# Kernel optimization log

Hardware: AMD Instinct MI355X
Metric: run time of the kernel (lower is better)

The kernel has to match this reference:

```python
import jax, jax.numpy as jnp
import numpy as np

N = 50000
E = 800000
D_IN = 256
D_H = 256


def setup_inputs() -> dict:
    key = jax.random.key(0)
    ks = jax.random.split(key, 8)
    x = jax.random.normal(ks[0], (N, D_IN), dtype=jnp.float32)
    W1 = jax.random.normal(ks[1], (D_H, D_IN), dtype=jnp.float32) * (1.0 / np.sqrt(D_IN))
    b1 = jnp.zeros((D_H,), dtype=jnp.float32)
    W2 = jax.random.normal(ks[2], (D_H, D_H), dtype=jnp.float32) * (1.0 / np.sqrt(D_H))
    b2 = jnp.zeros((D_H,), dtype=jnp.float32)
    gamma = jnp.ones((D_H,), dtype=jnp.float32)
    beta = jnp.zeros((D_H,), dtype=jnp.float32)
    adj_values = jax.random.uniform(ks[3], (E,), dtype=jnp.float32)
    rows = jax.random.randint(ks[4], (E,), 0, N, dtype=jnp.int64)
    cols = jax.random.randint(ks[5], (E,), 0, N, dtype=jnp.int64)
    adj_indices = jnp.stack([rows, cols], axis=0)
    return {"x": x, "W1": W1, "b1": b1, "W2": W2, "b2": b2,
            "gamma": gamma, "beta": beta, "adj_values": adj_values,
            "adj_indices": adj_indices}


def _spmm(adj_indices, adj_values, h, n):
    # out[i] = sum_j A[i, j] * h[j]; COO row=indices[0], col=indices[1]
    rows, cols = adj_indices[0], adj_indices[1]
    msgs = adj_values[:, None] * h[cols]          # [E, D]
    return jax.ops.segment_sum(msgs, rows, num_segments=n)


def _layernorm(h, gamma, beta, eps=1e-5):
    mu = jnp.mean(h, axis=-1, keepdims=True)
    var = jnp.var(h, axis=-1, keepdims=True)
    return (h - mu) * jax.lax.rsqrt(var + eps) * gamma + beta


def reference(x, W1, b1, W2, b2, gamma, beta, adj_values, adj_indices):
    n = x.shape[0]
    h = x @ W1.T + b1
    h = _spmm(adj_indices, adj_values, h, n)
    h = jax.nn.gelu(h, approximate=False)
    h = h @ W2.T + b2
    h = _spmm(adj_indices, adj_values, h, n)
    h = jax.nn.gelu(h, approximate=False)
    h = _layernorm(h + x[:, :h.shape[1]], gamma, beta)
    return h
```

## Files before the change

kernel.cpp:

```cpp
#include <hip/hip_runtime.h>
#include <math.h>

#define DH 256
#define CAP 64

typedef _Float16 f16x4 __attribute__((ext_vector_type(4)));
typedef _Float16 f16x8 __attribute__((ext_vector_type(8)));
typedef __fp16 fp16x2 __attribute__((ext_vector_type(2)));
typedef float f32x4 __attribute__((ext_vector_type(4)));

__device__ __forceinline__ float gelu_exact(float v) {
    return 0.5f * v * (1.0f + erff(v * 0.70710678118654752f));
}

__device__ __forceinline__ unsigned short f2h_bits(float f) {
    _Float16 h = (_Float16)f;
    return __builtin_bit_cast(unsigned short, h);
}

__device__ __forceinline__ _Float16 bits2h(unsigned short u) {
    return __builtin_bit_cast(_Float16, u);
}

__device__ __forceinline__ unsigned pk2h(float a, float b) {
    fp16x2 r = __builtin_amdgcn_cvt_pkrtz(a, b);
    return __builtin_bit_cast(unsigned, r);
}

__device__ __forceinline__ void async_copy16(const void* g, void* l) {
    __builtin_amdgcn_global_load_lds(
        (const __attribute__((address_space(1))) void*)g,
        (__attribute__((address_space(3))) void*)l, 16, 0, 0);
}

__global__ void prep_kernel(const float* __restrict__ W1, const float* __restrict__ W2,
                            unsigned short* __restrict__ W1h, unsigned short* __restrict__ W2h,
                            int* __restrict__ cnt, int n) {
    const int WV = DH * DH / 4;
    int gid = blockIdx.x * blockDim.x + threadIdx.x;
    if (gid < 2 * WV) {
        const float* src = (gid < WV) ? W1 : W2;
        unsigned short* dst = (gid < WV) ? W1h : W2h;
        int i = (gid < WV) ? gid : gid - WV;
        float4 v = *(const float4*)(src + (size_t)i * 4);
        uint2 o;
        o.x = pk2h(v.x, v.y);
        o.y = pk2h(v.z, v.w);
        *(uint2*)(dst + (size_t)i * 4) = o;
    } else {
        int i = (gid - 2 * WV) * 4;
        if (i < n) {
            int4 z = {0, 0, 0, 0};
            if (i + 4 <= n) *(int4*)(cnt + i) = z;
            else for (int k = i; k < n; ++k) cnt[k] = 0;
        }
    }
}

__global__ void bucket_kernel(const int* __restrict__ idx, const float* __restrict__ vals,
                              int* __restrict__ cnt, unsigned* __restrict__ cvb, int E) {
    int e = blockIdx.x * blockDim.x + threadIdx.x;
    if (e >= E) return;
    int r = idx[e];
    int c = idx[E + e];
    float v = vals[e];
    int p = atomicAdd(&cnt[r], 1);
    if (p < CAP) {
        cvb[(size_t)r * CAP + p] = ((unsigned)c << 16) | (unsigned)f2h_bits(v);
    }
}

template<bool AF32>
__global__ __launch_bounds__(512) void gemm_mfma_kernel(
        const void* __restrict__ Ap, const unsigned short* __restrict__ B,
        const float* __restrict__ bias, unsigned short* __restrict__ C, int M) {
    __shared__ char smem[49152];
    const int tid  = threadIdx.x;
    const int lane = tid & 63;
    const int wid  = tid >> 6;
    const int m0   = blockIdx.x * 128;
    const int wm   = wid >> 2;
    const int wn   = wid & 3;
    const int l15  = lane & 15, l4 = lane >> 4;

    auto stage = [&](int buf, int k0) {
        char* sA = smem + buf * 24576;
        char* sB = sA + 8192;
        {
            int t = tid;
            int row = t >> 2;
            int sw  = (t & 3) ^ (row & 3);
            int gra = m0 + row; if (gra >= M) gra = M - 1;
            if (AF32) {
                const float* a32 = (const float*)Ap + (size_t)gra * DH + k0 + sw * 8;
                float4 lo = *(const float4*)a32;
                float4 hi = *(const float4*)(a32 + 4);
                uint4 pk;
                pk.x = pk2h(lo.x, lo.y);
                pk.y = pk2h(lo.z, lo.w);
                pk.z = pk2h(hi.x, hi.y);
                pk.w = pk2h(hi.z, hi.w);
                *(uint4*)(sA + (size_t)t * 16) = pk;
            } else {
                async_copy16((const unsigned short*)Ap + (size_t)gra * DH + k0 + sw * 8,
                             sA + ((size_t)(wid * 64)) * 16);
            }
        }
        #pragma unroll
        for (int k = 0; k < 2; ++k) {
            int t = k * 512 + tid;
            int row = t >> 2;
            int sw  = (t & 3) ^ (row & 3);
            async_copy16(B + (size_t)row * DH + k0 + sw * 8,
                         sB + ((size_t)(k * 512 + wid * 64)) * 16);
        }
    };

    f32x4 acc[4][4] = {};

    stage(0, 0);
    __syncthreads();

    #pragma unroll
    for (int t = 0; t < 8; ++t) {
        if (t < 7) stage((t + 1) & 1, (t + 1) * 32);

        char* sA = smem + (t & 1) * 24576;
        char* sB = sA + 8192;
        f16x8 af[4], bfg[4];
        #pragma unroll
        for (int f = 0; f < 4; ++f) {
            int ra = wm * 64 + f * 16 + l15;
            int rb = wn * 64 + f * 16 + l15;
            int ca = (l4 ^ (ra & 3)) * 16;
            int cb = (l4 ^ (rb & 3)) * 16;
            af[f]  = *(const f16x8*)(sA + ra * 64 + ca);
            bfg[f] = *(const f16x8*)(sB + rb * 64 + cb);
        }
        #pragma unroll
        for (int fm = 0; fm < 4; ++fm)
            #pragma unroll
            for (int fn = 0; fn < 4; ++fn)
                acc[fm][fn] = __builtin_amdgcn_mfma_f32_16x16x32_f16(af[fm], bfg[fn], acc[fm][fn], 0, 0, 0);

        __syncthreads();
    }

    #pragma unroll
    for (int fn = 0; fn < 4; ++fn) {
        float bb = bias[wn * 64 + fn * 16 + l15];
        #pragma unroll
        for (int fm = 0; fm < 4; ++fm) {
            int mrow = m0 + wm * 64 + fm * 16 + l4 * 4;
            unsigned short* cp = C + (size_t)mrow * DH + wn * 64 + fn * 16 + l15;
            #pragma unroll
            for (int r = 0; r < 4; ++r) {
                if (mrow + r < M) cp[(size_t)r * DH] = f2h_bits(acc[fm][fn][r] + bb);
            }
        }
    }
}

template<int MODE>
__global__ __launch_bounds__(256) void spmm_kernel(
        const _Float16* __restrict__ h, const int* __restrict__ cnt,
        const unsigned* __restrict__ cvb, const float* __restrict__ xres,
        const float* __restrict__ gamma, const float* __restrict__ beta,
        void* __restrict__ outp, int n) {
    const int lane = threadIdx.x & 63;
    const int row = blockIdx.x * 4 + (threadIdx.x >> 6);
    if (row >= n) return;
    int deg = cnt[row]; if (deg > CAP) deg = CAP;
    const unsigned* cb = cvb + (size_t)row * CAP;

    f16x4 accA = {}, accB = {};
    int j = 0;
    for (; j + 4 <= deg; j += 4) {
        uint4 e = *(const uint4*)(cb + j);
        f16x4 p0 = *(const f16x4*)(h + (size_t)(e.x >> 16) * DH + lane * 4);
        f16x4 p1 = *(const f16x4*)(h + (size_t)(e.y >> 16) * DH + lane * 4);
        f16x4 p2 = *(const f16x4*)(h + (size_t)(e.z >> 16) * DH + lane * 4);
        f16x4 p3 = *(const f16x4*)(h + (size_t)(e.w >> 16) * DH + lane * 4);
        _Float16 v0 = bits2h((unsigned short)(e.x & 0xFFFFu));
        _Float16 v1 = bits2h((unsigned short)(e.y & 0xFFFFu));
        _Float16 v2 = bits2h((unsigned short)(e.z & 0xFFFFu));
        _Float16 v3 = bits2h((unsigned short)(e.w & 0xFFFFu));
        accA += p0 * v0; accB += p1 * v1;
        accA += p2 * v2; accB += p3 * v3;
    }
    for (; j < deg; ++j) {
        unsigned e = cb[j];
        f16x4 p0 = *(const f16x4*)(h + (size_t)(e >> 16) * DH + lane * 4);
        _Float16 v0 = bits2h((unsigned short)(e & 0xFFFFu));
        accA += p0 * v0;
    }

    float ax = (float)accA[0] + (float)accB[0];
    float ay = (float)accA[1] + (float)accB[1];
    float az = (float)accA[2] + (float)accB[2];
    float aw = (float)accA[3] + (float)accB[3];

    ax = gelu_exact(ax); ay = gelu_exact(ay); az = gelu_exact(az); aw = gelu_exact(aw);

    if (MODE == 1) {
        float4 xr = *(const float4*)(xres + (size_t)row * DH + lane * 4);
        ax += xr.x; ay += xr.y; az += xr.z; aw += xr.w;
        float s  = ax + ay + az + aw;
        float s2 = ax * ax + ay * ay + az * az + aw * aw;
        #pragma unroll
        for (int off = 32; off > 0; off >>= 1) {
            s  += __shfl_xor(s,  off);
            s2 += __shfl_xor(s2, off);
        }
        float mu  = s * (1.0f / 256.0f);
        float var = s2 * (1.0f / 256.0f) - mu * mu;
        float rs  = rsqrtf(var + 1e-5f);
        float4 g  = *(const float4*)(gamma + lane * 4);
        float4 bt = *(const float4*)(beta + lane * 4);
        float4 o;
        o.x = (ax - mu) * rs * g.x + bt.x;
        o.y = (ay - mu) * rs * g.y + bt.y;
        o.z = (az - mu) * rs * g.z + bt.z;
        o.w = (aw - mu) * rs * g.w + bt.w;
        *(float4*)((float*)outp + (size_t)row * DH + lane * 4) = o;
    } else {
        uint2 pk;
        pk.x = pk2h(ax, ay);
        pk.y = pk2h(az, aw);
        *(uint2*)((_Float16*)outp + (size_t)row * DH + lane * 4) = pk;
    }
}

extern "C" void kernel_launch(void* const* d_in, const int* in_sizes, int n_in,
                              void* d_out, int out_size, void* d_ws, size_t ws_size,
                              hipStream_t stream) {
    const float* x     = (const float*)d_in[0];
    const float* W1    = (const float*)d_in[1];
    const float* b1    = (const float*)d_in[2];
    const float* W2    = (const float*)d_in[3];
    const float* b2    = (const float*)d_in[4];
    const float* gamma = (const float*)d_in[5];
    const float* beta  = (const float*)d_in[6];
    const float* avals = (const float*)d_in[7];
    const int*   aidx  = (const int*)d_in[8];

    const int n = in_sizes[0] / DH;
    const int e = in_sizes[7];
    float* out = (float*)d_out;

    _Float16* g1h = (_Float16*)d_out;

    char* ws = (char*)d_ws;
    size_t off = 0;
    _Float16* hb = (_Float16*)(ws + off);              off += (size_t)n * DH * 2;
    off = (off + 255) & ~(size_t)255;
    unsigned short* W1h = (unsigned short*)(ws + off); off += (size_t)DH * DH * 2;
    off = (off + 255) & ~(size_t)255;
    unsigned short* W2h = (unsigned short*)(ws + off); off += (size_t)DH * DH * 2;
    off = (off + 255) & ~(size_t)255;
    int* cnt = (int*)(ws + off);                       off += (size_t)n * sizeof(int);
    off = (off + 255) & ~(size_t)255;
    unsigned* cvb = (unsigned*)(ws + off);             off += (size_t)n * CAP * sizeof(unsigned);

    const int gemm_gx = (n + 127) / 128;
    const int prep_items = 2 * (DH * DH / 4) + (n + 3) / 4;

    prep_kernel<<<(prep_items + 255) / 256, 256, 0, stream>>>(W1, W2, W1h, W2h, cnt, n);
    bucket_kernel<<<(e + 255) / 256, 256, 0, stream>>>(aidx, avals, cnt, cvb, e);

    gemm_mfma_kernel<true><<<gemm_gx, 512, 0, stream>>>(x, W1h, b1, (unsigned short*)hb, n);

    spmm_kernel<0><<<(n + 3) / 4, 256, 0, stream>>>(
        hb, cnt, cvb, nullptr, nullptr, nullptr, g1h, n);

    gemm_mfma_kernel<false><<<gemm_gx, 512, 0, stream>>>(g1h, W2h, b2, (unsigned short*)hb, n);

    spmm_kernel<1><<<(n + 3) / 4, 256, 0, stream>>>(
        hb, cnt, cvb, x, gamma, beta, out, n);
}
```

Measured before the change: 216.2 us.

## Drop prep kernel and LDS staging; load GEMM operands directly from global

Removes the separate prep kernel that converted W1/W2 to fp16 and zeroed the bucket counters. The counter zeroing moves into the first GEMM kernel, and the weights are now read as fp32 and converted inline. The GEMM also drops its double-buffered LDS staging and barriers, so each wave loads its A and B fragments straight from global memory into registers. This saves one launch and the LDS traffic, but every wave now reloads and reconverts fp32 weights with strided, partially coalesced global loads, and nothing overlaps those loads with the MFMA work.

After: 308.7 us. 42.8% more time.

```diff
diff --git a/kernel.cpp b/kernel.cpp
--- a/kernel.cpp
+++ b/kernel.cpp
@@ -25,36 +25,6 @@
 __device__ __forceinline__ unsigned pk2h(float a, float b) {
     fp16x2 r = __builtin_amdgcn_cvt_pkrtz(a, b);
     return __builtin_bit_cast(unsigned, r);
-}
-
-__device__ __forceinline__ void async_copy16(const void* g, void* l) {
-    __builtin_amdgcn_global_load_lds(
-        (const __attribute__((address_space(1))) void*)g,
-        (__attribute__((address_space(3))) void*)l, 16, 0, 0);
-}
-
-__global__ void prep_kernel(const float* __restrict__ W1, const float* __restrict__ W2,
-                            unsigned short* __restrict__ W1h, unsigned short* __restrict__ W2h,
-                            int* __restrict__ cnt, int n) {
-    const int WV = DH * DH / 4;
-    int gid = blockIdx.x * blockDim.x + threadIdx.x;
-    if (gid < 2 * WV) {
-        const float* src = (gid < WV) ? W1 : W2;
-        unsigned short* dst = (gid < WV) ? W1h : W2h;
-        int i = (gid < WV) ? gid : gid - WV;
-        float4 v = *(const float4*)(src + (size_t)i * 4);
-        uint2 o;
-        o.x = pk2h(v.x, v.y);
-        o.y = pk2h(v.z, v.w);
-        *(uint2*)(dst + (size_t)i * 4) = o;
-    } else {
-        int i = (gid - 2 * WV) * 4;
-        if (i < n) {
-            int4 z = {0, 0, 0, 0};
-            if (i + 4 <= n) *(int4*)(cnt + i) = z;
-            else for (int k = i; k < n; ++k) cnt[k] = 0;
-        }
-    }
 }
 
 __global__ void bucket_kernel(const int* __restrict__ idx, const float* __restrict__ vals,
@@ -72,10 +42,16 @@
 
 template<bool AF32>
 __global__ __launch_bounds__(512) void gemm_mfma_kernel(
-        const void* __restrict__ Ap, const unsigned short* __restrict__ B,
-        const float* __restrict__ bias, unsigned short* __restrict__ C, int M) {
-    __shared__ char smem[49152];
+        const void* __restrict__ Ap, const float* __restrict__ Bf,
+        const float* __restrict__ bias, unsigned short* __restrict__ C,
+        int* __restrict__ cnt_zero, int M) {
     const int tid  = threadIdx.x;
+
+    if (cnt_zero) {
+        int zi = blockIdx.x * 512 + tid;
+        if (zi < M) cnt_zero[zi] = 0;
+    }
+
     const int lane = tid & 63;
     const int wid  = tid >> 6;
     const int m0   = blockIdx.x * 128;
@@ -83,67 +59,46 @@
     const int wn   = wid & 3;
     const int l15  = lane & 15, l4 = lane >> 4;
 
-    auto stage = [&](int buf, int k0) {
-        char* sA = smem + buf * 24576;
-        char* sB = sA + 8192;
-        {
-            int t = tid;
-            int row = t >> 2;
-            int sw  = (t & 3) ^ (row & 3);
-            int gra = m0 + row; if (gra >= M) gra = M - 1;
-            if (AF32) {
-                const float* a32 = (const float*)Ap + (size_t)gra * DH + k0 + sw * 8;
-                float4 lo = *(const float4*)a32;
-                float4 hi = *(const float4*)(a32 + 4);
-                uint4 pk;
-                pk.x = pk2h(lo.x, lo.y);
-                pk.y = pk2h(lo.z, lo.w);
-                pk.z = pk2h(hi.x, hi.y);
-                pk.w = pk2h(hi.z, hi.w);
-                *(uint4*)(sA + (size_t)t * 16) = pk;
-            } else {
-                async_copy16((const unsigned short*)Ap + (size_t)gra * DH + k0 + sw * 8,
-                             sA + ((size_t)(wid * 64)) * 16);
-            }
-        }
-        #pragma unroll
-        for (int k = 0; k < 2; ++k) {
-            int t = k * 512 + tid;
-            int row = t >> 2;
-            int sw  = (t & 3) ^ (row & 3);
-            async_copy16(B + (size_t)row * DH + k0 + sw * 8,
-                         sB + ((size_t)(k * 512 + wid * 64)) * 16);
-        }
-    };
+    int ra[4], rb[4];
+    #pragma unroll
+    for (int f = 0; f < 4; ++f) {
+        int r = m0 + wm * 64 + f * 16 + l15;
+        ra[f] = (r < M) ? r : (M - 1);
+        rb[f] = wn * 64 + f * 16 + l15;
+    }
 
     f32x4 acc[4][4] = {};
-
-    stage(0, 0);
-    __syncthreads();
 
     #pragma unroll
     for (int t = 0; t < 8; ++t) {
-        if (t < 7) stage((t + 1) & 1, (t + 1) * 32);
-
-        char* sA = smem + (t & 1) * 24576;
-        char* sB = sA + 8192;
-        f16x8 af[4], bfg[4];
+        const int k0 = t * 32 + l4 * 8;
+        f16x8 af[4], bf[4];
         #pragma unroll
         for (int f = 0; f < 4; ++f) {
-            int ra = wm * 64 + f * 16 + l15;
-            int rb = wn * 64 + f * 16 + l15;
-            int ca = (l4 ^ (ra & 3)) * 16;
-            int cb = (l4 ^ (rb & 3)) * 16;
-            af[f]  = *(const f16x8*)(sA + ra * 64 + ca);
-            bfg[f] = *(const f16x8*)(sB + rb * 64 + cb);
+            if (AF32) {
+                const float* ap = (const float*)Ap + (size_t)ra[f] * DH + k0;
+                float4 lo = *(const float4*)ap;
+                float4 hi = *(const float4*)(ap + 4);
+                uint4 pk;
+                pk.x = pk2h(lo.x, lo.y); pk.y = pk2h(lo.z, lo.w);
+                pk.z = pk2h(hi.x, hi.y); pk.w = pk2h(hi.z, hi.w);
+                af[f] = __builtin_bit_cast(f16x8, pk);
+            } else {
+                af[f] = *(const f16x8*)((const _Float16*)Ap + (size_t)ra[f] * DH + k0);
+            }
+            const float* bp = Bf + (size_t)rb[f] * DH + k0;
+            float4 blo = *(const float4*)bp;
+            float4 bhi = *(const float4*)(bp + 4);
+            uint4 pkb;
+            pkb.x = pk2h(blo.x, blo.y); pkb.y = pk2h(blo.z, blo.w);
+            pkb.z = pk2h(bhi.x, bhi.y); pkb.w = pk2h(bhi.z, bhi.w);
+            bf[f] = __builtin_bit_cast(f16x8, pkb);
         }
         #pragma unroll
         for (int fm = 0; fm < 4; ++fm)
             #pragma unroll
             for (int fn = 0; fn < 4; ++fn)
-                acc[fm][fn] = __builtin_amdgcn_mfma_f32_16x16x32_f16(af[fm], bfg[fn], acc[fm][fn], 0, 0, 0);
-
-        __syncthreads();
+                acc[fm][fn] = __builtin_amdgcn_mfma_f32_16x16x32_f16(af[fm], bf[fn], acc[fm][fn], 0, 0, 0);
     }
 
     #pragma unroll
@@ -254,26 +209,20 @@
     size_t off = 0;
     _Float16* hb = (_Float16*)(ws + off);              off += (size_t)n * DH * 2;
     off = (off + 255) & ~(size_t)255;
-    unsigned short* W1h = (unsigned short*)(ws + off); off += (size_t)DH * DH * 2;
-    off = (off + 255) & ~(size_t)255;
-    unsigned short* W2h = (unsigned short*)(ws + off); off += (size_t)DH * DH * 2;
-    off = (off + 255) & ~(size_t)255;
     int* cnt = (int*)(ws + off);                       off += (size_t)n * sizeof(int);
     off = (off + 255) & ~(size_t)255;
     unsigned* cvb = (unsigned*)(ws + off);             off += (size_t)n * CAP * sizeof(unsigned);
 
     const int gemm_gx = (n + 127) / 128;
-    const int prep_items = 2 * (DH * DH / 4) + (n + 3) / 4;
-
-    prep_kernel<<<(prep_items + 255) / 256, 256, 0, stream>>>(W1, W2, W1h, W2h, cnt, n);
+
+    gemm_mfma_kernel<true><<<gemm_gx, 512, 0, stream>>>(x, W1, b1, (unsigned short*)hb, cnt, n);
+
     bucket_kernel<<<(e + 255) / 256, 256, 0, stream>>>(aidx, avals, cnt, cvb, e);
-
-    gemm_mfma_kernel<true><<<gemm_gx, 512, 0, stream>>>(x, W1h, b1, (unsigned short*)hb, n);
 
     spmm_kernel<0><<<(n + 3) / 4, 256, 0, stream>>>(
         hb, cnt, cvb, nullptr, nullptr, nullptr, g1h, n);
 
-    gemm_mfma_kernel<false><<<gemm_gx, 512, 0, stream>>>(g1h, W2h, b2, (unsigned short*)hb, n);
+    gemm_mfma_kernel<false><<<gemm_gx, 512, 0, stream>>>(g1h, W2, b2, (unsigned short*)hb, nullptr, n);
 
     spmm_kernel<1><<<(n + 3) / 4, 256, 0, stream>>>(
         hb, cnt, cvb, x, gamma, beta, out, n);
```

## Triple-buffer GEMM k-loop with register-prefetched A and explicit vmcnt waits

Applied to the files above, without the earlier changes.

Restructures the MFMA GEMM main loop into a three-stage software pipeline. B tiles (and f16 A tiles) are async-copied into a triple-buffered LDS ring two k-steps ahead, while f32 A tiles are prefetched into registers and converted to f16 just before use. __syncthreads is replaced by explicit s_waitcnt vmcnt counts plus a raw s_barrier, and launch bounds now ask for 4 blocks per CU. This hides global-load latency at the cost of more LDS (64-72KB) and more registers, which may limit occupancy. Correctness depends on hand-counted vmcnt values and a single barrier per step.

Result: no change. 218.3 us, median of 2 (+1.0%).

```diff
diff --git a/kernel.cpp b/kernel.cpp
--- a/kernel.cpp
+++ b/kernel.cpp
@@ -71,10 +71,12 @@
 }
 
 template<bool AF32>
-__global__ __launch_bounds__(512) void gemm_mfma_kernel(
-        const void* __restrict__ Ap, const unsigned short* __restrict__ B,
+__global__ __launch_bounds__(512, 4) void gemm_mfma_kernel(
+        const void* __restrict__ Ap, const unsigned short* __restrict__ Bh,
         const float* __restrict__ bias, unsigned short* __restrict__ C, int M) {
-    __shared__ char smem[49152];
+    __shared__ char smem[AF32 ? 65536 : 73728];
+    char* bufB = smem;
+    char* bufA = smem + 49152;
     const int tid  = threadIdx.x;
     const int lane = tid & 63;
     const int wid  = tid >> 6;
@@ -83,67 +85,85 @@
     const int wn   = wid & 3;
     const int l15  = lane & 15, l4 = lane >> 4;
 
-    auto stage = [&](int buf, int k0) {
-        char* sA = smem + buf * 24576;
-        char* sB = sA + 8192;
-        {
-            int t = tid;
-            int row = t >> 2;
-            int sw  = (t & 3) ^ (row & 3);
-            int gra = m0 + row; if (gra >= M) gra = M - 1;
-            if (AF32) {
-                const float* a32 = (const float*)Ap + (size_t)gra * DH + k0 + sw * 8;
-                float4 lo = *(const float4*)a32;
-                float4 hi = *(const float4*)(a32 + 4);
-                uint4 pk;
-                pk.x = pk2h(lo.x, lo.y);
-                pk.y = pk2h(lo.z, lo.w);
-                pk.z = pk2h(hi.x, hi.y);
-                pk.w = pk2h(hi.z, hi.w);
-                *(uint4*)(sA + (size_t)t * 16) = pk;
-            } else {
-                async_copy16((const unsigned short*)Ap + (size_t)gra * DH + k0 + sw * 8,
-                             sA + ((size_t)(wid * 64)) * 16);
-            }
-        }
-        #pragma unroll
-        for (int k = 0; k < 2; ++k) {
-            int t = k * 512 + tid;
-            int row = t >> 2;
-            int sw  = (t & 3) ^ (row & 3);
-            async_copy16(B + (size_t)row * DH + k0 + sw * 8,
-                         sB + ((size_t)(k * 512 + wid * 64)) * 16);
-        }
+    const int arow = tid >> 2;
+    const int asw  = (tid & 3) ^ (arow & 3);
+    int gra = m0 + arow; if (gra >= M) gra = M - 1;
+    const float*     a32 = (const float*)Ap + (size_t)gra * DH + asw * 8;
+    const _Float16*  a16 = (const _Float16*)Ap + (size_t)gra * DH + asw * 8;
+    const unsigned short* b0p = Bh + (size_t)arow * DH + asw * 8;
+    const unsigned short* b1p = Bh + (size_t)(arow + 128) * DH + asw * 8;
+
+    float4 aLo[2], aHi[2];
+
+    auto stageB = [&](int buf, int k0) {
+        char* sB = bufB + buf * 16384;
+        async_copy16(b0p + k0, sB + (size_t)(wid * 64) * 16);
+        async_copy16(b1p + k0, sB + (size_t)(512 + wid * 64) * 16);
     };
+    auto stageA16 = [&](int buf, int k0) {
+        async_copy16(a16 + k0, bufA + buf * 8192 + (size_t)(wid * 64) * 16);
+    };
 
     f32x4 acc[4][4] = {};
 
-    stage(0, 0);
-    __syncthreads();
+    if constexpr (AF32) {
+        aLo[0] = *(const float4*)(a32 + 0);  aHi[0] = *(const float4*)(a32 + 4);
+    } else {
+        stageA16(0, 0);
+    }
+    stageB(0, 0);
+    if constexpr (AF32) {
+        aLo[1] = *(const float4*)(a32 + 32); aHi[1] = *(const float4*)(a32 + 36);
+    } else {
+        stageA16(1, 32);
+    }
+    stageB(1, 32);
 
     #pragma unroll
     for (int t = 0; t < 8; ++t) {
-        if (t < 7) stage((t + 1) & 1, (t + 1) * 32);
-
-        char* sA = smem + (t & 1) * 24576;
-        char* sB = sA + 8192;
-        f16x8 af[4], bfg[4];
+        if (t == 7)      { asm volatile("s_waitcnt vmcnt(0)" ::: "memory"); }
+        else if (AF32)   { asm volatile("s_waitcnt vmcnt(4)" ::: "memory"); }
+        else             { asm volatile("s_waitcnt vmcnt(3)" ::: "memory"); }
+        if constexpr (AF32) {
+            uint4 pk;
+            pk.x = pk2h(aLo[t & 1].x, aLo[t & 1].y);
+            pk.y = pk2h(aLo[t & 1].z, aLo[t & 1].w);
+            pk.z = pk2h(aHi[t & 1].x, aHi[t & 1].y);
+            pk.w = pk2h(aHi[t & 1].z, aHi[t & 1].w);
+            *(uint4*)(bufA + (t & 1) * 8192 + (size_t)tid * 16) = pk;
+            asm volatile("s_waitcnt lgkmcnt(0)" ::: "memory");
+        }
+        __builtin_amdgcn_s_barrier();
+        __builtin_amdgcn_sched_barrier(0);
+
+        char* sA = bufA + (AF32 ? (t & 1) : (t % 3)) * 8192;
+        char* sB = bufB + (t % 3) * 16384;
+        f16x8 af[4], bf[4];
         #pragma unroll
         for (int f = 0; f < 4; ++f) {
             int ra = wm * 64 + f * 16 + l15;
             int rb = wn * 64 + f * 16 + l15;
             int ca = (l4 ^ (ra & 3)) * 16;
             int cb = (l4 ^ (rb & 3)) * 16;
-            af[f]  = *(const f16x8*)(sA + ra * 64 + ca);
-            bfg[f] = *(const f16x8*)(sB + rb * 64 + cb);
+            af[f] = *(const f16x8*)(sA + ra * 64 + ca);
+            bf[f] = *(const f16x8*)(sB + rb * 64 + cb);
         }
         #pragma unroll
         for (int fm = 0; fm < 4; ++fm)
             #pragma unroll
             for (int fn = 0; fn < 4; ++fn)
-                acc[fm][fn] = __builtin_amdgcn_mfma_f32_16x16x32_f16(af[fm], bfg[fn], acc[fm][fn], 0, 0, 0);
-
-        __syncthreads();
+                acc[fm][fn] = __builtin_amdgcn_mfma_f32_16x16x32_f16(af[fm], bf[fn], acc[fm][fn], 0, 0, 0);
+
+        if (t < 6) {
+            int k0 = (t + 2) * 32;
+            if constexpr (AF32) {
+                aLo[t & 1] = *(const float4*)(a32 + k0);
+                aHi[t & 1] = *(const float4*)(a32 + k0 + 4);
+            } else {
+                stageA16((t + 2) % 3, k0);
+            }
+            stageB((t + 2) % 3, k0);
+        }
     }
 
     #pragma unroll
```
